# Performance work log

Measured on AMD Instinct MI355X. Metric: run time of the kernel, lower is better.

## Reference

```python
import jax, jax.numpy as jnp
import numpy as np

EPS = 1e-12


def _l2norm(x):
    # F.normalize(x, dim=1): x / max(||x||, eps)
    n = jnp.sqrt(jnp.sum(x * x, axis=1, keepdims=True))
    return x / jnp.maximum(n, EPS)


def _remove_diag(x):
    # x: [n, n] -> [n, n-1], dropping the diagonal (matches x[~eye].view(n, -1))
    n = x.shape[0]
    row = jnp.arange(n)[:, None]
    base = jnp.arange(n - 1)[None, :]
    cols = jnp.where(base < row, base, base + 1)  # column indices != row index
    return jnp.take_along_axis(x, cols, axis=1)


def _lid_mle(data, reference, k):
    # pairwise euclidean distances [n_data, n_ref]
    d2 = (jnp.sum(data * data, axis=1)[:, None]
          + jnp.sum(reference * reference, axis=1)[None, :]
          - 2.0 * data @ reference.T)
    dist = jnp.sqrt(jnp.maximum(d2, 0.0))
    # k+1 smallest distances (index 0 is the self-distance since data subset of reference)
    neg_top, _ = jax.lax.top_k(-dist, k + 1)
    d = -neg_top[:, 1:]  # [n, k], ascending, self excluded
    # MLE LID estimator: -k / sum_i log(d_i / d_k)
    return -k / jnp.sum(jnp.log(d / d[:, -1:] + EPS), axis=1)


def _byol_loss(p, z):
    z = jax.lax.stop_gradient(z)
    return 2.0 - 2.0 * jnp.sum(_l2norm(p) * _l2norm(z), axis=1)


def _track_logits(o0, o1):
    b = o0.shape[0]
    l00 = _remove_diag(jnp.einsum('nc,mc->nm', o0, o0))
    l01 = jnp.einsum('nc,mc->nm', o0, o1)
    l10 = jnp.einsum('nc,mc->nm', o1, o0)
    l11 = _remove_diag(jnp.einsum('nc,mc->nm', o1, o1))
    logits = jnp.concatenate([
        jnp.concatenate([l01, l00], axis=1),
        jnp.concatenate([l10, l11], axis=1)], axis=0)  # [2b, 2b-1]
    labels = jnp.tile(jnp.arange(b, dtype=jnp.int32), 2)
    return logits, labels


def setup_inputs() -> dict:
    key = jax.random.key(0)
    ks = jax.random.split(key, 9)
    B, Dfe, Dp, C = 4096, 2048, 256, 1000
    return {
        'fe_0': jax.random.normal(ks[0], (B, Dfe), jnp.float32),
        'fe_1': jax.random.normal(ks[1], (B, Dfe), jnp.float32),
        'p_0': jax.random.normal(ks[2], (B, Dp), jnp.float32),
        'p_1': jax.random.normal(ks[3], (B, Dp), jnp.float32),
        'z_0': jax.random.normal(ks[4], (B, Dp), jnp.float32),
        'z_1': jax.random.normal(ks[5], (B, Dp), jnp.float32),
        'cls_0': jax.random.normal(ks[6], (B, C), jnp.float32),
        'cls_1': jax.random.normal(ks[7], (B, C), jnp.float32),
        'online_labels': jax.random.randint(ks[8], (B,), 0, C, jnp.int32),
    }


def reference(fe_0, fe_1, p_0, p_1, z_0, z_1, cls_0, cls_1, online_labels):
    # BYOL symmetric loss
    main_loss = jnp.mean(_byol_loss(p_0, z_1) + _byol_loss(p_1, z_0))
    # online linear-probe cross-entropy on concatenated views
    cls = jnp.concatenate([cls_0, cls_1], axis=0)
    labels2 = jnp.concatenate([online_labels, online_labels], axis=0)
    logp = jax.nn.log_softmax(cls, axis=1)
    online_loss = -jnp.mean(jnp.take_along_axis(logp, labels2[:, None], axis=1)[:, 0])
    # LID tracking on backbone features (no-grad in original)
    fe = jnp.concatenate([fe_0, fe_1], axis=0)
    lids32 = _lid_mle(fe, fe, 32)
    lids512 = _lid_mle(fe, fe, 512)
    # contrastive-style logit tracking on normalized predictor outputs
    logits, labels = _track_logits(_l2norm(p_0), _l2norm(p_1))
    return main_loss, online_loss, logits, labels, lids32, lids512
```

## Files before the change

kernel.cpp:

```cpp
#include <hip/hip_runtime.h>
#include <math.h>

typedef __bf16 bf16;
typedef __bf16 bf16x8 __attribute__((ext_vector_type(8)));
typedef __bf16 bf16x4 __attribute__((ext_vector_type(4)));
typedef float f32x4 __attribute__((ext_vector_type(4)));

#define NROW 8192
#define BHALF 4096
#define DFE 2048
#define DP 256
#define NCLS 1000

#define LOGITS_N 8191
#define OUT_LOGITS 2
#define OUT_LABELS (2 + 8192 * 8191)
#define OUT_LIDS32 (OUT_LABELS + 8192)
#define OUT_LIDS512 (OUT_LIDS32 + 8192)

__device__ inline void gload16(const bf16* g, bf16* l) {
    __builtin_amdgcn_global_load_lds((const __attribute__((address_space(1))) void*)g,
                                     (__attribute__((address_space(3))) void*)l, 16, 0, 0);
}

__global__ __launch_bounds__(256) void init_kernel(float* out) {
    int i = blockIdx.x * 256 + threadIdx.x;
    if (i < 2) out[i] = 0.f;
    if (i < NROW) out[(size_t)OUT_LABELS + i] = (float)(i & (BHALF - 1));
}

__global__ __launch_bounds__(256) void split_fe_kernel(const float* __restrict__ fe0,
                                                       const float* __restrict__ fe1,
                                                       bf16* __restrict__ feh,
                                                       bf16* __restrict__ fel,
                                                       float* __restrict__ norms) {
    int row = blockIdx.x, tid = threadIdx.x;
    const float* src = (row < BHALF) ? fe0 + (size_t)row * DFE
                                     : fe1 + (size_t)(row - BHALF) * DFE;
    float ss = 0.f;
#pragma unroll
    for (int pass = 0; pass < 2; ++pass) {
        int c = (pass * 256 + tid) * 4;
        float4 v = *(const float4*)(src + c);
        ss += v.x * v.x + v.y * v.y + v.z * v.z + v.w * v.w;
        bf16 h0 = (bf16)v.x, h1 = (bf16)v.y, h2 = (bf16)v.z, h3 = (bf16)v.w;
        bf16 l0 = (bf16)(v.x - (float)h0), l1 = (bf16)(v.y - (float)h1);
        bf16 l2 = (bf16)(v.z - (float)h2), l3 = (bf16)(v.w - (float)h3);
        bf16x4 hv = {h0, h1, h2, h3};
        bf16x4 lv = {l0, l1, l2, l3};
        *(bf16x4*)(feh + (size_t)row * DFE + c) = hv;
        *(bf16x4*)(fel + (size_t)row * DFE + c) = lv;
    }
#pragma unroll
    for (int off = 32; off; off >>= 1) ss += __shfl_down(ss, off);
    __shared__ float red[4];
    if ((tid & 63) == 0) red[tid >> 6] = ss;
    __syncthreads();
    if (tid == 0) norms[row] = red[0] + red[1] + red[2] + red[3];
}

__global__ __launch_bounds__(256) void norm_split_p_kernel(const float* __restrict__ p0,
                                                           const float* __restrict__ p1,
                                                           bf16* __restrict__ oh) {
    int row = blockIdx.x, tid = threadIdx.x;
    const float* src = (row < BHALF) ? p0 + (size_t)row * DP
                                     : p1 + (size_t)(row - BHALF) * DP;
    float x = src[tid];
    float ss = x * x;
#pragma unroll
    for (int off = 32; off; off >>= 1) ss += __shfl_down(ss, off);
    __shared__ float red[4];
    if ((tid & 63) == 0) red[tid >> 6] = ss;
    __syncthreads();
    float tot = red[0] + red[1] + red[2] + red[3];
    float rn = 1.f / fmaxf(sqrtf(tot), 1e-12f);
    oh[(size_t)row * DP + tid] = (bf16)(x * rn);
}

__device__ inline float dot4(float4 a, float4 b) {
    return a.x * b.x + a.y * b.y + a.z * b.z + a.w * b.w;
}

__global__ __launch_bounds__(256) void byol_kernel(const float* __restrict__ p0,
                                                   const float* __restrict__ p1,
                                                   const float* __restrict__ z0,
                                                   const float* __restrict__ z1,
                                                   float* out) {
    int tid = threadIdx.x, wave = tid >> 6, lane = tid & 63;
    int row = blockIdx.x * 4 + wave;
    size_t base = (size_t)row * DP + lane * 4;
    float4 a0 = *(const float4*)(p0 + base);
    float4 b0 = *(const float4*)(z1 + base);
    float4 a1 = *(const float4*)(p1 + base);
    float4 b1 = *(const float4*)(z0 + base);
    float pp0 = dot4(a0, a0), zz0 = dot4(b0, b0), pz0 = dot4(a0, b0);
    float pp1 = dot4(a1, a1), zz1 = dot4(b1, b1), pz1 = dot4(a1, b1);
#pragma unroll
    for (int off = 32; off; off >>= 1) {
        pp0 += __shfl_down(pp0, off); zz0 += __shfl_down(zz0, off); pz0 += __shfl_down(pz0, off);
        pp1 += __shfl_down(pp1, off); zz1 += __shfl_down(zz1, off); pz1 += __shfl_down(pz1, off);
    }
    __shared__ float red[4];
    if (lane == 0) {
        float c0 = pz0 / (fmaxf(sqrtf(pp0), 1e-12f) * fmaxf(sqrtf(zz0), 1e-12f));
        float c1 = pz1 / (fmaxf(sqrtf(pp1), 1e-12f) * fmaxf(sqrtf(zz1), 1e-12f));
        red[wave] = (2.f - 2.f * c0) + (2.f - 2.f * c1);
    }
    __syncthreads();
    if (tid == 0) atomicAdd(out, (red[0] + red[1] + red[2] + red[3]) * (1.f / 4096.f));
}

__global__ __launch_bounds__(256) void online_kernel(const float* __restrict__ cls0,
                                                     const float* __restrict__ cls1,
                                                     const int* __restrict__ labels,
                                                     float* out) {
    int tid = threadIdx.x, wave = tid >> 6, lane = tid & 63;
    int row = blockIdx.x * 4 + wave;
    const float* src = (row < BHALF) ? cls0 + (size_t)row * NCLS
                                     : cls1 + (size_t)(row - BHALF) * NCLS;
    int lbl = labels[row & (BHALF - 1)];
    float xs[16];
    float mx = -INFINITY;
#pragma unroll
    for (int j = 0; j < 16; ++j) {
        int c = lane + j * 64;
        xs[j] = (c < NCLS) ? src[c] : -INFINITY;
        mx = fmaxf(mx, xs[j]);
    }
#pragma unroll
    for (int off = 32; off; off >>= 1) mx = fmaxf(mx, __shfl_xor(mx, off));
    float se = 0.f;
#pragma unroll
    for (int j = 0; j < 16; ++j) se += expf(xs[j] - mx);
#pragma unroll
    for (int off = 32; off; off >>= 1) se += __shfl_xor(se, off);
    __shared__ float red[4];
    if (lane == 0) red[wave] = src[lbl] - mx - logf(se);
    __syncthreads();
    if (tid == 0) atomicAdd(out + 1, -(red[0] + red[1] + red[2] + red[3]) * (1.f / 8192.f));
}

__global__ __launch_bounds__(256) void gemm_kernel(const bf16* __restrict__ Hp,
                                                   const bf16* __restrict__ Lp,
                                                   int K, int nchunks, int mode,
                                                   const float* __restrict__ norms,
                                                   float* __restrict__ d2,
                                                   float* __restrict__ outlog) {
    __shared__ bf16 As[128 * 64];
    __shared__ bf16 Bs[128 * 64];
    int tid = threadIdx.x, lane = tid & 63, wave = tid >> 6;
    int tm, tn;
    if (mode == 0) {
        int L = blockIdx.x;
        int t = (int)((sqrtf(8.f * (float)L + 1.f) - 1.f) * 0.5f);
        while ((t + 1) * (t + 2) / 2 <= L) ++t;
        while (t * (t + 1) / 2 > L) --t;
        tn = t;
        tm = L - t * (t + 1) / 2;
    } else {
        tm = blockIdx.x & 63;
        tn = blockIdx.x >> 6;
    }

    int wr = wave >> 1, wc = wave & 1;
    int lrow = lane & 15, lquad = lane >> 4, r7 = lrow & 7;

    int rsub = lane >> 3;
    int grp = lane & 7;
    int lg = grp ^ rsub;

    int aoff[4], boff[4];
#pragma unroll
    for (int t = 0; t < 4; ++t) {
        aoff[t] = (((wr * 64 + t * 16 + lrow) * 64) + (lquad ^ r7) * 8) * 2;
        boff[t] = (((wc * 64 + t * 16 + lrow) * 64) + (lquad ^ r7) * 8) * 2;
    }
    const char* Asb = (const char*)As;
    const char* Bsb = (const char*)Bs;

    f32x4 acc[4][4];
    f32x4 zz = {0.f, 0.f, 0.f, 0.f};
#pragma unroll
    for (int i = 0; i < 4; ++i)
#pragma unroll
        for (int j = 0; j < 4; ++j) acc[i][j] = zz;

    bf16* Al = As + wave * 32 * 64;
    bf16* Bl = Bs + wave * 32 * 64;

    for (int chunk = 0; chunk < nchunks; ++chunk) {
        const bf16* Ab = (chunk == 1) ? Lp : Hp;
        const bf16* Bb = (chunk == 2) ? Lp : Hp;
        const bf16* Ag = Ab + (size_t)(tm * 128 + wave * 32 + rsub) * K + lg * 8;
        const bf16* Bg = Bb + (size_t)(tn * 128 + wave * 32 + rsub) * K + lg * 8;
        for (int k0 = 0; k0 < K; k0 += 64) {
#pragma unroll
            for (int t = 0; t < 4; ++t) {
                gload16(Ag + (size_t)t * 8 * K + k0, Al + t * 8 * 64);
                gload16(Bg + (size_t)t * 8 * K + k0, Bl + t * 8 * 64);
            }
            __syncthreads();
#pragma unroll
            for (int ks = 0; ks < 2; ++ks) {
                bf16x8 af[4], bf_[4];
#pragma unroll
                for (int t = 0; t < 4; ++t) af[t] = *(const bf16x8*)(Asb + (aoff[t] ^ (ks * 64)));
#pragma unroll
                for (int t = 0; t < 4; ++t) bf_[t] = *(const bf16x8*)(Bsb + (boff[t] ^ (ks * 64)));
#pragma unroll
                for (int i = 0; i < 4; ++i)
#pragma unroll
                    for (int j = 0; j < 4; ++j)
                        acc[i][j] = __builtin_amdgcn_mfma_f32_16x16x32_bf16(af[i], bf_[j], acc[i][j], 0, 0, 0);
            }
            __syncthreads();
        }
    }

    int rowbase = tm * 128 + wr * 64;
    int colbase = tn * 128 + wc * 64;
    if (mode == 0) {
#pragma unroll
        for (int i = 0; i < 4; ++i) {
#pragma unroll
            for (int e = 0; e < 4; ++e) {
                int grow = rowbase + i * 16 + lquad * 4 + e;
                float na = norms[grow];
#pragma unroll
                for (int j = 0; j < 4; ++j) {
                    int gcol = colbase + j * 16 + lrow;
                    float v = na + norms[gcol] - 2.f * acc[i][j][e];
                    d2[(size_t)grow * NROW + gcol] = fmaxf(v, 0.f);
                }
            }
        }
    } else {
#pragma unroll
        for (int i = 0; i < 4; ++i) {
#pragma unroll
            for (int j = 0; j < 4; ++j) {
#pragma unroll
                for (int e = 0; e < 4; ++e) {
                    int r = rowbase + i * 16 + lquad * 4 + e;
                    int c = colbase + j * 16 + lrow;
                    int oc = 0;
                    bool skip = false;
                    if (r < BHALF) {
                        if (c >= BHALF) oc = c - BHALF;
                        else if (c == r) skip = true;
                        else oc = BHALF + (c < r ? c : c - 1);
                    } else {
                        int rp = r - BHALF;
                        if (c < BHALF) oc = c;
                        else {
                            int cp = c - BHALF;
                            if (cp == rp) skip = true;
                            else oc = BHALF + (cp < rp ? cp : cp - 1);
                        }
                    }
                    if (!skip) outlog[(size_t)r * LOGITS_N + oc] = acc[i][j][e];
                }
            }
        }
    }
}

__global__ __launch_bounds__(256) void mirror_kernel(float* __restrict__ d2) {
    int bj = blockIdx.x, bi = blockIdx.y;
    if (bi < bj) return;
    __shared__ float t[32][33];
    int tx = threadIdx.x & 31, ty = threadIdx.x >> 5;
#pragma unroll
    for (int r = 0; r < 32; r += 8)
        t[r + ty][tx] = d2[(size_t)(bj * 32 + r + ty) * NROW + bi * 32 + tx];
    __syncthreads();
#pragma unroll
    for (int r = 0; r < 32; r += 8) {
        int gi = bi * 32 + r + ty, gj = bj * 32 + tx;
        if (gi > gj) d2[(size_t)gi * NROW + gj] = t[tx][r + ty];
    }
}

__global__ __launch_bounds__(256) void select_kernel(const float* __restrict__ d2,
                                                     float* __restrict__ out) {
    int row = blockIdx.x, tid = threadIdx.x;
    int lane = tid & 63, wave = tid >> 6;
    const float4* drow4 = (const float4*)(d2 + (size_t)row * NROW);
    unsigned v[32];
#pragma unroll
    for (int j = 0; j < 8; ++j) {
        int idx4 = j * 256 + tid;
        float4 f = drow4[idx4];
        int c0 = idx4 * 4;
        v[j * 4 + 0] = (c0 == row) ? 0xFFFFFFFFu : __float_as_uint(f.x);
        v[j * 4 + 1] = (c0 + 1 == row) ? 0xFFFFFFFFu : __float_as_uint(f.y);
        v[j * 4 + 2] = (c0 + 2 == row) ? 0xFFFFFFFFu : __float_as_uint(f.z);
        v[j * 4 + 3] = (c0 + 3 == row) ? 0xFFFFFFFFu : __float_as_uint(f.w);
    }
    __shared__ unsigned redu[8];
    __shared__ unsigned dec;
    unsigned p1 = 0, p2 = 0;
    for (int bit = 31; bit >= 0; --bit) {
        unsigned c1 = p1 | (1u << bit), c2 = p2 | (1u << bit);
        unsigned n1 = 0, n2 = 0;
#pragma unroll
        for (int j = 0; j < 32; ++j) { n1 += (v[j] < c1); n2 += (v[j] < c2); }
#pragma unroll
        for (int off = 32; off; off >>= 1) {
            n1 += __shfl_down(n1, off);
            n2 += __shfl_down(n2, off);
        }
        if (lane == 0) { redu[wave * 2] = n1; redu[wave * 2 + 1] = n2; }
        __syncthreads();
        if (tid == 0) {
            unsigned t1 = redu[0] + redu[2] + redu[4] + redu[6];
            unsigned t2 = redu[1] + redu[3] + redu[5] + redu[7];
            dec = ((t1 < 32u) ? 1u : 0u) | ((t2 < 512u) ? 2u : 0u);
        }
        __syncthreads();
        unsigned d = dec;
        if (d & 1u) p1 = c1;
        if (d & 2u) p2 = c2;
    }
    float dk1 = sqrtf(__uint_as_float(p1));
    float dk2 = sqrtf(__uint_as_float(p2));
    float s1 = 0.f, s2 = 0.f;
#pragma unroll
    for (int j = 0; j < 32; ++j) {
        unsigned b = v[j];
        if (b < p2) {
            float d = sqrtf(__uint_as_float(b));
            s2 += logf(d / dk2 + 1e-12f);
            if (b < p1) s1 += logf(d / dk1 + 1e-12f);
        }
    }
#pragma unroll
    for (int off = 32; off; off >>= 1) {
        s1 += __shfl_down(s1, off);
        s2 += __shfl_down(s2, off);
    }
    __shared__ float redf[8];
    if (lane == 0) { redf[wave * 2] = s1; redf[wave * 2 + 1] = s2; }
    __syncthreads();
    if (tid == 0) {
        float t1 = redf[0] + redf[2] + redf[4] + redf[6];
        float t2 = redf[1] + redf[3] + redf[5] + redf[7];
        out[(size_t)OUT_LIDS32 + row] = -32.f / t1;
        out[(size_t)OUT_LIDS512 + row] = -512.f / t2;
    }
}

extern "C" void kernel_launch(void* const* d_in, const int* in_sizes, int n_in,
                              void* d_out, int out_size, void* d_ws, size_t ws_size,
                              hipStream_t stream) {
    const float* fe0 = (const float*)d_in[0];
    const float* fe1 = (const float*)d_in[1];
    const float* p0 = (const float*)d_in[2];
    const float* p1 = (const float*)d_in[3];
    const float* z0 = (const float*)d_in[4];
    const float* z1 = (const float*)d_in[5];
    const float* cls0 = (const float*)d_in[6];
    const float* cls1 = (const float*)d_in[7];
    const int* labels = (const int*)d_in[8];
    float* out = (float*)d_out;

    char* ws = (char*)d_ws;
    float* D2 = (float*)ws;
    bf16* FEH = (bf16*)(ws + 268435456UL);
    bf16* FEL = (bf16*)(ws + 268435456UL + 33554432UL);
    bf16* OH = (bf16*)(ws + 268435456UL + 2 * 33554432UL);
    float* NORMS = (float*)(ws + 268435456UL + 2 * 33554432UL + 4194304UL);

    init_kernel<<<32, 256, 0, stream>>>(out);
    split_fe_kernel<<<8192, 256, 0, stream>>>(fe0, fe1, FEH, FEL, NORMS);
    norm_split_p_kernel<<<8192, 256, 0, stream>>>(p0, p1, OH);
    byol_kernel<<<1024, 256, 0, stream>>>(p0, p1, z0, z1, out);
    online_kernel<<<2048, 256, 0, stream>>>(cls0, cls1, labels, out);
    gemm_kernel<<<2080, 256, 0, stream>>>(FEH, FEL, DFE, 3, 0, NORMS, D2, nullptr);
    mirror_kernel<<<dim3(256, 256), 256, 0, stream>>>(D2);
    select_kernel<<<8192, 256, 0, stream>>>(D2, out);
    gemm_kernel<<<4096, 256, 0, stream>>>(OH, OH, DP, 1, 1, nullptr, nullptr, out + OUT_LOGITS);
}
```

Before: 1.318 ms.

## Pipeline merged 256x128 GEMM and make LID select one wave per row

Both GEMMs run in a single launch of 512-thread blocks with 256x128 tiles. K-slices are double-buffered in LDS with explicit vmcnt waits, raised MFMA priority and a swizzled tile order, so global loads overlap with compute. The select kernel now gives each row to a single wave holding 128 values in registers. It first finds the common high-bit prefix across the row, so the radix search skips those bits, and it no longer needs block-level barriers. In exchange, register pressure and pipelining complexity are much higher, and the tile mapping must still cover the upper triangle exactly.

Result: faster. 1.287 ms (-2.4%).

```diff
diff --git a/kernel.cpp b/kernel.cpp
--- a/kernel.cpp
+++ b/kernel.cpp
@@ -17,6 +17,9 @@
 #define OUT_LABELS (2 + 8192 * 8191)
 #define OUT_LIDS32 (OUT_LABELS + 8192)
 #define OUT_LIDS512 (OUT_LIDS32 + 8192)
+
+#define G0TILES 1056
+#define G1TILES 2048
 
 __device__ inline void gload16(const bf16* g, bf16* l) {
     __builtin_amdgcn_global_load_lds((const __attribute__((address_space(1))) void*)g,
@@ -140,43 +143,48 @@
     if (tid == 0) atomicAdd(out + 1, -(red[0] + red[1] + red[2] + red[3]) * (1.f / 8192.f));
 }
 
-__global__ __launch_bounds__(256) void gemm_kernel(const bf16* __restrict__ Hp,
-                                                   const bf16* __restrict__ Lp,
-                                                   int K, int nchunks, int mode,
-                                                   const float* __restrict__ norms,
-                                                   float* __restrict__ d2,
-                                                   float* __restrict__ outlog) {
-    __shared__ bf16 As[128 * 64];
-    __shared__ bf16 Bs[128 * 64];
+__device__ inline void stage_half(const bf16* __restrict__ mat, int Kd, int rowbase,
+                                  int k0, bf16* lds, int wave, int rsub, int lg) {
+#pragma unroll
+    for (int q = 0; q < 2; ++q)
+        gload16(mat + (size_t)(rowbase + q * 64 + wave * 8 + rsub) * Kd + k0 + lg * 8,
+                lds + (q * 64 + wave * 8) * 64);
+}
+
+__global__ __launch_bounds__(512, 2) void gemm_kernel(const bf16* __restrict__ Hp,
+                                                      const bf16* __restrict__ Lp,
+                                                      const bf16* __restrict__ OHp,
+                                                      const float* __restrict__ norms,
+                                                      float* __restrict__ d2,
+                                                      float* __restrict__ outlog) {
+    __shared__ bf16 sm[2][24576];
     int tid = threadIdx.x, lane = tid & 63, wave = tid >> 6;
-    int tm, tn;
-    if (mode == 0) {
-        int L = blockIdx.x;
-        int t = (int)((sqrtf(8.f * (float)L + 1.f) - 1.f) * 0.5f);
-        while ((t + 1) * (t + 2) / 2 <= L) ++t;
-        while (t * (t + 1) / 2 > L) --t;
-        tn = t;
-        tm = L - t * (t + 1) / 2;
+    int wr = wave >> 1, wc = wave & 1;
+    int lrow = lane & 15, lquad = lane >> 4, r7 = lrow & 7, pg = lquad ^ r7;
+    int rsub = lane >> 3, grp = lane & 7, lg = grp ^ rsub;
+
+    int bid = blockIdx.x;
+    int mode, tm, tn, ksh;
+    const bf16 *Hmat, *Lmat;
+    int Kd;
+    if (bid < G0TILES) {
+        mode = 0;
+        int sw = (bid & 7) * (G0TILES / 8) + (bid >> 3);
+        int i = 0;
+        while ((i + 1) * (65 - (i + 1)) <= sw) ++i;
+        tm = i;
+        tn = 2 * i + (sw - i * (65 - i));
+        Hmat = Hp; Lmat = Lp; Kd = DFE; ksh = 5;
     } else {
-        tm = blockIdx.x & 63;
-        tn = blockIdx.x >> 6;
-    }
-
-    int wr = wave >> 1, wc = wave & 1;
-    int lrow = lane & 15, lquad = lane >> 4, r7 = lrow & 7;
-
-    int rsub = lane >> 3;
-    int grp = lane & 7;
-    int lg = grp ^ rsub;
-
-    int aoff[4], boff[4];
-#pragma unroll
-    for (int t = 0; t < 4; ++t) {
-        aoff[t] = (((wr * 64 + t * 16 + lrow) * 64) + (lquad ^ r7) * 8) * 2;
-        boff[t] = (((wc * 64 + t * 16 + lrow) * 64) + (lquad ^ r7) * 8) * 2;
-    }
-    const char* Asb = (const char*)As;
-    const char* Bsb = (const char*)Bs;
+        mode = 1;
+        int id = bid - G0TILES;
+        int sw = (id & 7) * (G1TILES / 8) + (id >> 3);
+        tm = sw & 31; tn = sw >> 5;
+        Hmat = OHp; Lmat = OHp; Kd = DP; ksh = 2;
+    }
+    int NT = (mode == 0 ? 3 : 1) << ksh;
+    int kmask = (1 << ksh) - 1;
+    int arow0 = tm * 256, brow0 = tn * 128;
 
     f32x4 acc[4][4];
     f32x4 zz = {0.f, 0.f, 0.f, 0.f};
@@ -185,50 +193,100 @@
 #pragma unroll
         for (int j = 0; j < 4; ++j) acc[i][j] = zz;
 
-    bf16* Al = As + wave * 32 * 64;
-    bf16* Bl = Bs + wave * 32 * 64;
-
-    for (int chunk = 0; chunk < nchunks; ++chunk) {
-        const bf16* Ab = (chunk == 1) ? Lp : Hp;
-        const bf16* Bb = (chunk == 2) ? Lp : Hp;
-        const bf16* Ag = Ab + (size_t)(tm * 128 + wave * 32 + rsub) * K + lg * 8;
-        const bf16* Bg = Bb + (size_t)(tn * 128 + wave * 32 + rsub) * K + lg * 8;
-        for (int k0 = 0; k0 < K; k0 += 64) {
-#pragma unroll
-            for (int t = 0; t < 4; ++t) {
-                gload16(Ag + (size_t)t * 8 * K + k0, Al + t * 8 * 64);
-                gload16(Bg + (size_t)t * 8 * K + k0, Bl + t * 8 * 64);
+    stage_half(Hmat, Kd, arow0, 0, sm[0], wave, rsub, lg);
+    stage_half(Hmat, Kd, brow0, 0, sm[0] + 16384, wave, rsub, lg);
+    stage_half(Hmat, Kd, arow0 + 128, 0, sm[0] + 8192, wave, rsub, lg);
+    stage_half(Hmat, Kd, arow0, 64, sm[1], wave, rsub, lg);
+    stage_half(Hmat, Kd, brow0, 64, sm[1] + 16384, wave, rsub, lg);
+    asm volatile("s_waitcnt vmcnt(6)" ::: "memory");
+    __builtin_amdgcn_s_barrier();
+
+    bf16x8 bfr[4][2];
+    for (int gt = 0; gt < NT; ++gt) {
+        int cur = gt & 1;
+        const char* Sb = (const char*)sm[cur];
+        const bf16 *A1m = Hmat, *A2m = Hmat, *B2m = Hmat;
+        int k01 = 0, k02 = 0;
+        if (gt + 1 < NT) {
+            int nt = gt + 1, ch = nt >> ksh;
+            k01 = (nt & kmask) * 64;
+            A1m = (ch == 1) ? Lmat : Hmat;
+        }
+        if (gt + 2 < NT) {
+            int nt = gt + 2, ch = nt >> ksh;
+            k02 = (nt & kmask) * 64;
+            A2m = (ch == 1) ? Lmat : Hmat;
+            B2m = (ch == 2) ? Lmat : Hmat;
+        }
+
+        bf16x8 af[2][2];
+#pragma unroll
+        for (int ii = 0; ii < 2; ++ii) {
+            int off = ((ii * 4 + wr) * 16 + lrow) * 128 + pg * 16;
+            af[ii][0] = *(const bf16x8*)(Sb + off);
+            af[ii][1] = *(const bf16x8*)(Sb + (off ^ 64));
+        }
+#pragma unroll
+        for (int j = 0; j < 4; ++j) {
+            int off = 32768 + ((j * 2 + wc) * 16 + lrow) * 128 + pg * 16;
+            bfr[j][0] = *(const bf16x8*)(Sb + off);
+            bfr[j][1] = *(const bf16x8*)(Sb + (off ^ 64));
+        }
+        if (gt + 1 < NT)
+            stage_half(A1m, Kd, arow0 + 128, k01, sm[cur ^ 1] + 8192, wave, rsub, lg);
+        __builtin_amdgcn_s_barrier();
+        asm volatile("s_waitcnt lgkmcnt(0)" ::: "memory");
+        __builtin_amdgcn_sched_barrier(0);
+        __builtin_amdgcn_s_setprio(1);
+#pragma unroll
+        for (int ii = 0; ii < 2; ++ii)
+#pragma unroll
+            for (int j = 0; j < 4; ++j) {
+                acc[ii][j] = __builtin_amdgcn_mfma_f32_16x16x32_bf16(af[ii][0], bfr[j][0], acc[ii][j], 0, 0, 0);
+                acc[ii][j] = __builtin_amdgcn_mfma_f32_16x16x32_bf16(af[ii][1], bfr[j][1], acc[ii][j], 0, 0, 0);
             }
-            __syncthreads();
-#pragma unroll
-            for (int ks = 0; ks < 2; ++ks) {
-                bf16x8 af[4], bf_[4];
-#pragma unroll
-                for (int t = 0; t < 4; ++t) af[t] = *(const bf16x8*)(Asb + (aoff[t] ^ (ks * 64)));
-#pragma unroll
-                for (int t = 0; t < 4; ++t) bf_[t] = *(const bf16x8*)(Bsb + (boff[t] ^ (ks * 64)));
-#pragma unroll
-                for (int i = 0; i < 4; ++i)
-#pragma unroll
-                    for (int j = 0; j < 4; ++j)
-                        acc[i][j] = __builtin_amdgcn_mfma_f32_16x16x32_bf16(af[i], bf_[j], acc[i][j], 0, 0, 0);
+        __builtin_amdgcn_s_setprio(0);
+        if (gt + 1 < NT) asm volatile("s_waitcnt vmcnt(6)" ::: "memory");
+        else             asm volatile("s_waitcnt vmcnt(0)" ::: "memory");
+        __builtin_amdgcn_s_barrier();
+
+#pragma unroll
+        for (int ii = 0; ii < 2; ++ii) {
+            int off = (((ii + 2) * 4 + wr) * 16 + lrow) * 128 + pg * 16;
+            af[ii][0] = *(const bf16x8*)(Sb + off);
+            af[ii][1] = *(const bf16x8*)(Sb + (off ^ 64));
+        }
+        if (gt + 2 < NT) {
+            stage_half(A2m, Kd, arow0, k02, sm[cur], wave, rsub, lg);
+            stage_half(B2m, Kd, brow0, k02, sm[cur] + 16384, wave, rsub, lg);
+        }
+        __builtin_amdgcn_s_barrier();
+        asm volatile("s_waitcnt lgkmcnt(0)" ::: "memory");
+        __builtin_amdgcn_sched_barrier(0);
+        __builtin_amdgcn_s_setprio(1);
+#pragma unroll
+        for (int ii = 0; ii < 2; ++ii)
+#pragma unroll
+            for (int j = 0; j < 4; ++j) {
+                acc[ii + 2][j] = __builtin_amdgcn_mfma_f32_16x16x32_bf16(af[ii][0], bfr[j][0], acc[ii + 2][j], 0, 0, 0);
+                acc[ii + 2][j] = __builtin_amdgcn_mfma_f32_16x16x32_bf16(af[ii][1], bfr[j][1], acc[ii + 2][j], 0, 0, 0);
             }
-            __syncthreads();
-        }
-    }
-
-    int rowbase = tm * 128 + wr * 64;
-    int colbase = tn * 128 + wc * 64;
+        __builtin_amdgcn_s_setprio(0);
+        if (gt + 2 < NT)      asm volatile("s_waitcnt vmcnt(6)" ::: "memory");
+        else if (gt + 1 < NT) asm volatile("s_waitcnt vmcnt(2)" ::: "memory");
+        __builtin_amdgcn_s_barrier();
+    }
+
     if (mode == 0) {
 #pragma unroll
         for (int i = 0; i < 4; ++i) {
 #pragma unroll
             for (int e = 0; e < 4; ++e) {
-                int grow = rowbase + i * 16 + lquad * 4 + e;
+                int grow = arow0 + (i * 4 + wr) * 16 + lquad * 4 + e;
                 float na = norms[grow];
 #pragma unroll
                 for (int j = 0; j < 4; ++j) {
-                    int gcol = colbase + j * 16 + lrow;
+                    int gcol = tn * 128 + (j * 2 + wc) * 16 + lrow;
                     float v = na + norms[gcol] - 2.f * acc[i][j][e];
                     d2[(size_t)grow * NROW + gcol] = fmaxf(v, 0.f);
                 }
@@ -241,8 +299,8 @@
             for (int j = 0; j < 4; ++j) {
 #pragma unroll
                 for (int e = 0; e < 4; ++e) {
-                    int r = rowbase + i * 16 + lquad * 4 + e;
-                    int c = colbase + j * 16 + lrow;
+                    int r = arow0 + (i * 4 + wr) * 16 + lquad * 4 + e;
+                    int c = tn * 128 + (j * 2 + wc) * 16 + lrow;
                     int oc = 0;
                     bool skip = false;
                     if (r < BHALF) {
@@ -283,50 +341,55 @@
 
 __global__ __launch_bounds__(256) void select_kernel(const float* __restrict__ d2,
                                                      float* __restrict__ out) {
-    int row = blockIdx.x, tid = threadIdx.x;
-    int lane = tid & 63, wave = tid >> 6;
+    int wave = threadIdx.x >> 6, lane = threadIdx.x & 63;
+    int row = blockIdx.x * 4 + wave;
     const float4* drow4 = (const float4*)(d2 + (size_t)row * NROW);
-    unsigned v[32];
-#pragma unroll
-    for (int j = 0; j < 8; ++j) {
-        int idx4 = j * 256 + tid;
+    unsigned v[128];
+    unsigned andv = 0xFFFFFFFFu, orv = 0u;
+#pragma unroll
+    for (int j = 0; j < 32; ++j) {
+        int idx4 = j * 64 + lane;
         float4 f = drow4[idx4];
         int c0 = idx4 * 4;
-        v[j * 4 + 0] = (c0 == row) ? 0xFFFFFFFFu : __float_as_uint(f.x);
-        v[j * 4 + 1] = (c0 + 1 == row) ? 0xFFFFFFFFu : __float_as_uint(f.y);
-        v[j * 4 + 2] = (c0 + 2 == row) ? 0xFFFFFFFFu : __float_as_uint(f.z);
-        v[j * 4 + 3] = (c0 + 3 == row) ? 0xFFFFFFFFu : __float_as_uint(f.w);
-    }
-    __shared__ unsigned redu[8];
-    __shared__ unsigned dec;
-    unsigned p1 = 0, p2 = 0;
-    for (int bit = 31; bit >= 0; --bit) {
+        unsigned u0 = __float_as_uint(f.x), u1 = __float_as_uint(f.y);
+        unsigned u2 = __float_as_uint(f.z), u3 = __float_as_uint(f.w);
+        bool s0 = (c0 == row), s1 = (c0 + 1 == row), s2 = (c0 + 2 == row), s3 = (c0 + 3 == row);
+        v[j * 4 + 0] = s0 ? 0xFFFFFFFFu : u0;
+        v[j * 4 + 1] = s1 ? 0xFFFFFFFFu : u1;
+        v[j * 4 + 2] = s2 ? 0xFFFFFFFFu : u2;
+        v[j * 4 + 3] = s3 ? 0xFFFFFFFFu : u3;
+        andv &= (s0 ? 0xFFFFFFFFu : u0); orv |= (s0 ? 0u : u0);
+        andv &= (s1 ? 0xFFFFFFFFu : u1); orv |= (s1 ? 0u : u1);
+        andv &= (s2 ? 0xFFFFFFFFu : u2); orv |= (s2 ? 0u : u2);
+        andv &= (s3 ? 0xFFFFFFFFu : u3); orv |= (s3 ? 0u : u3);
+    }
+#pragma unroll
+    for (int off = 32; off; off >>= 1) {
+        andv &= __shfl_xor(andv, off);
+        orv |= __shfl_xor(orv, off);
+    }
+    unsigned diff = andv ^ orv;
+    int msb = 31 - __clz((int)(diff | 1u));
+    unsigned common = (msb == 31) ? 0u : (andv & (0xFFFFFFFFu << (msb + 1)));
+    unsigned p1 = common, p2 = common;
+    for (int bit = msb; bit >= 0; --bit) {
         unsigned c1 = p1 | (1u << bit), c2 = p2 | (1u << bit);
         unsigned n1 = 0, n2 = 0;
 #pragma unroll
-        for (int j = 0; j < 32; ++j) { n1 += (v[j] < c1); n2 += (v[j] < c2); }
+        for (int j = 0; j < 128; ++j) { n1 += (v[j] < c1); n2 += (v[j] < c2); }
 #pragma unroll
         for (int off = 32; off; off >>= 1) {
-            n1 += __shfl_down(n1, off);
-            n2 += __shfl_down(n2, off);
-        }
-        if (lane == 0) { redu[wave * 2] = n1; redu[wave * 2 + 1] = n2; }
-        __syncthreads();
-        if (tid == 0) {
-            unsigned t1 = redu[0] + redu[2] + redu[4] + redu[6];
-            unsigned t2 = redu[1] + redu[3] + redu[5] + redu[7];
-            dec = ((t1 < 32u) ? 1u : 0u) | ((t2 < 512u) ? 2u : 0u);
-        }
-        __syncthreads();
-        unsigned d = dec;
-        if (d & 1u) p1 = c1;
-        if (d & 2u) p2 = c2;
+            n1 += __shfl_xor(n1, off);
+            n2 += __shfl_xor(n2, off);
+        }
+        if (n1 < 32u) p1 = c1;
+        if (n2 < 512u) p2 = c2;
     }
     float dk1 = sqrtf(__uint_as_float(p1));
     float dk2 = sqrtf(__uint_as_float(p2));
     float s1 = 0.f, s2 = 0.f;
 #pragma unroll
-    for (int j = 0; j < 32; ++j) {
+    for (int j = 0; j < 128; ++j) {
         unsigned b = v[j];
         if (b < p2) {
             float d = sqrtf(__uint_as_float(b));
@@ -336,17 +399,12 @@
     }
 #pragma unroll
     for (int off = 32; off; off >>= 1) {
-        s1 += __shfl_down(s1, off);
-        s2 += __shfl_down(s2, off);
-    }
-    __shared__ float redf[8];
-    if (lane == 0) { redf[wave * 2] = s1; redf[wave * 2 + 1] = s2; }
-    __syncthreads();
-    if (tid == 0) {
-        float t1 = redf[0] + redf[2] + redf[4] + redf[6];
-        float t2 = redf[1] + redf[3] + redf[5] + redf[7];
-        out[(size_t)OUT_LIDS32 + row] = -32.f / t1;
-        out[(size_t)OUT_LIDS512 + row] = -512.f / t2;
+        s1 += __shfl_xor(s1, off);
+        s2 += __shfl_xor(s2, off);
+    }
+    if (lane == 0) {
+        out[(size_t)OUT_LIDS32 + row] = -32.f / s1;
+        out[(size_t)OUT_LIDS512 + row] = -512.f / s2;
     }
 }
 
@@ -376,8 +434,7 @@
     norm_split_p_kernel<<<8192, 256, 0, stream>>>(p0, p1, OH);
     byol_kernel<<<1024, 256, 0, stream>>>(p0, p1, z0, z1, out);
     online_kernel<<<2048, 256, 0, stream>>>(cls0, cls1, labels, out);
-    gemm_kernel<<<2080, 256, 0, stream>>>(FEH, FEL, DFE, 3, 0, NORMS, D2, nullptr);
+    gemm_kernel<<<G0TILES + G1TILES, 512, 0, stream>>>(FEH, FEL, OH, NORMS, D2, out + OUT_LOGITS);
     mirror_kernel<<<dim3(256, 256), 256, 0, stream>>>(D2);
-    select_kernel<<<8192, 256, 0, stream>>>(D2, out);
-    gemm_kernel<<<4096, 256, 0, stream>>>(OH, OH, DP, 1, 1, nullptr, nullptr, out + OUT_LOGITS);
-}
+    select_kernel<<<2048, 256, 0, stream>>>(D2, out);
+}
```
